# Performance work log

Hardware: AMD Instinct MI355X
Metric: run time of the kernel (lower is better)

The kernel has to match this reference:

```python
import jax, jax.numpy as jnp
import numpy as np

T = 1024      # number of timesteps
B = 32768     # number of independent regions / batch elements
STEP = 0.5    # fixed Euler step size (self.step in the torch module)


def setup_inputs() -> dict:
    key = jax.random.key(0)
    k1, k2, k3, k4 = jax.random.split(key, 4)
    return {
        "initial": jax.random.uniform(k1, (4, B), dtype=jnp.float32),  # [S0,E0,I0,R0]
        "beta": jax.random.uniform(k2, (1,), dtype=jnp.float32),
        "gamma": jax.random.uniform(k3, (1,), dtype=jnp.float32),
        "sigma": jax.random.uniform(k4, (1,), dtype=jnp.float32),
        "t": T,
    }


def reference(initial, beta, gamma, sigma, t):
    # Faithful Euler SEIR stepping: each update uses the *previous* step's
    # values of all four compartments (matches the torch indexing with [n]).
    step = jnp.float32(STEP)
    b, g, s = beta[0], gamma[0], sigma[0]
    S0, E0, I0, R0 = initial[0], initial[1], initial[2], initial[3]  # each (B,)

    def body(carry, _):
        S, E, I, R = carry
        Sn = S - b * S * I * step
        En = E + (b * S * I - s * E) * step
        In = I + (s * E - g * I) * step
        Rn = R + g * I * step
        new = (Sn, En, In, Rn)
        return new, new

    _, traj = jax.lax.scan(body, (S0, E0, I0, R0), None, length=t - 1)
    # Prepend initial state; torch cats time-major per compartment -> (t*B,)
    Ss = jnp.concatenate([S0[None], traj[0]], axis=0).reshape(-1)
    Es = jnp.concatenate([E0[None], traj[1]], axis=0).reshape(-1)
    Is = jnp.concatenate([I0[None], traj[2]], axis=0).reshape(-1)
    Rs = jnp.concatenate([R0[None], traj[3]], axis=0).reshape(-1)
    return jnp.stack([Ss, Es, Is, Rs], axis=1)  # (t*B, 4)
```

## Files before the change

### kernel.cpp

```cpp
#include <hip/hip_runtime.h>

#define T_STEPS 1024
#define B_ELEMS 32768
#define STEP 0.5f

typedef float f32x4 __attribute__((ext_vector_type(4)));

__global__ __launch_bounds__(64) void seir_euler_kernel(
    const float* __restrict__ initial,
    const float* __restrict__ beta,
    const float* __restrict__ gamma,
    const float* __restrict__ sigma,
    f32x4* __restrict__ out,
    int T, int B)
{
    int b = blockIdx.x * blockDim.x + threadIdx.x;
    if (b >= B) return;

    const float bb = beta[0];
    const float gg = gamma[0];
    const float ss = sigma[0];

    float S = initial[0 * B + b];
    float E = initial[1 * B + b];
    float I = initial[2 * B + b];
    float R = initial[3 * B + b];

    f32x4 v0 = {S, E, I, R};
    __builtin_nontemporal_store(v0, &out[b]);

    size_t idx = (size_t)B + b;
    for (int n = 1; n < T; ++n, idx += B) {
        float bSI = bb * S * I;
        float sE  = ss * E;
        float gI  = gg * I;
        float Sn = S - bSI * STEP;
        float En = E + (bSI - sE) * STEP;
        float In = I + (sE - gI) * STEP;
        float Rn = R + gI * STEP;
        S = Sn; E = En; I = In; R = Rn;
        f32x4 v = {S, E, I, R};
        __builtin_nontemporal_store(v, &out[idx]);
    }
}

extern "C" void kernel_launch(void* const* d_in, const int* in_sizes, int n_in,
                              void* d_out, int out_size, void* d_ws, size_t ws_size,
                              hipStream_t stream)
{
    const float* initial = (const float*)d_in[0];
    const float* beta    = (const float*)d_in[1];
    const float* gamma   = (const float*)d_in[2];
    const float* sigma   = (const float*)d_in[3];
    f32x4* out = (f32x4*)d_out;

    const int B = B_ELEMS;
    const int block = 64;
    const int grid = (B + block - 1) / block;
    seir_euler_kernel<<<grid, block, 0, stream>>>(initial, beta, gamma, sigma,
                                                  out, T_STEPS, B);
}
```

Before: 92.37 us.

## Split timesteps across threads with redundant prefix recomputation for more parallelism

Each batch element is now handled by four threads, each owning a quarter of the timesteps. A thread first replays the Euler recurrence silently up to its chunk start, then writes its chunk. This raises the number of in-flight waves issuing stores, which were previously limited to one thread per element. The cost is redundant arithmetic for the prefix (up to three quarters of the steps for the last chunk), which adds load imbalance across threads.

Measured after the change: 103.4 us. 1.12x slower.

```diff
diff --git a/kernel.cpp b/kernel.cpp
--- a/kernel.cpp
+++ b/kernel.cpp
@@ -2,20 +2,22 @@
 
 #define T_STEPS 1024
 #define B_ELEMS 32768
+#define K_SPLIT 4
+#define NS (T_STEPS / K_SPLIT)
 #define STEP 0.5f
 
 typedef float f32x4 __attribute__((ext_vector_type(4)));
 
-__global__ __launch_bounds__(64) void seir_euler_kernel(
+__global__ __launch_bounds__(256) void seir_euler_kernel(
     const float* __restrict__ initial,
     const float* __restrict__ beta,
     const float* __restrict__ gamma,
     const float* __restrict__ sigma,
     f32x4* __restrict__ out,
-    int T, int B)
+    int B)
 {
-    int b = blockIdx.x * blockDim.x + threadIdx.x;
-    if (b >= B) return;
+    const int b = blockIdx.x * 64 + threadIdx.x;
+    const int c = threadIdx.y;
 
     const float bb = beta[0];
     const float gg = gamma[0];
@@ -26,11 +28,8 @@
     float I = initial[2 * B + b];
     float R = initial[3 * B + b];
 
-    f32x4 v0 = {S, E, I, R};
-    __builtin_nontemporal_store(v0, &out[b]);
-
-    size_t idx = (size_t)B + b;
-    for (int n = 1; n < T; ++n, idx += B) {
+    const int start = c * NS;
+    for (int n = 0; n < start; ++n) {
         float bSI = bb * S * I;
         float sE  = ss * E;
         float gI  = gg * I;
@@ -39,8 +38,21 @@
         float In = I + (sE - gI) * STEP;
         float Rn = R + gI * STEP;
         S = Sn; E = En; I = In; R = Rn;
+    }
+
+    size_t idx = (size_t)start * B + b;
+#pragma unroll 2
+    for (int n = 0; n < NS; ++n, idx += B) {
         f32x4 v = {S, E, I, R};
         __builtin_nontemporal_store(v, &out[idx]);
+        float bSI = bb * S * I;
+        float sE  = ss * E;
+        float gI  = gg * I;
+        float Sn = S - bSI * STEP;
+        float En = E + (bSI - sE) * STEP;
+        float In = I + (sE - gI) * STEP;
+        float Rn = R + gI * STEP;
+        S = Sn; E = En; I = In; R = Rn;
     }
 }
 
@@ -55,8 +67,7 @@
     f32x4* out = (f32x4*)d_out;
 
     const int B = B_ELEMS;
-    const int block = 64;
-    const int grid = (B + block - 1) / block;
-    seir_euler_kernel<<<grid, block, 0, stream>>>(initial, beta, gamma, sigma,
-                                                  out, T_STEPS, B);
+    dim3 block(64, K_SPLIT);
+    dim3 grid(B / 64);
+    seir_euler_kernel<<<grid, block, 0, stream>>>(initial, beta, gamma, sigma, out, B);
 }
```
